# Kernel optimization log

Measured on AMD Instinct MI355X. Metric: run time of the kernel, lower is better.

Reference implementation:

```python
import jax, jax.numpy as jnp
import numpy as np

B = 262144
IN_F = 64
OUT_F = 64
HID = 256
QUAT_IDX = np.array([0, 1, 2, 3])
NON_QUAT_IDX = np.array(sorted(set(range(OUT_F)) - set(QUAT_IDX.tolist())))
TRIU_R, TRIU_C = np.triu_indices(4)  # row-major order, matches torch.triu_indices


def setup_inputs() -> dict:
    key = jax.random.key(0)
    k0, k1, k2 = jax.random.split(key, 3)
    z = jax.random.normal(k0, (B, IN_F), dtype=jnp.float32)
    W1 = jax.random.normal(k1, (IN_F, HID), dtype=jnp.float32) * (1.0 / np.sqrt(IN_F))
    b1 = jnp.zeros((HID,), dtype=jnp.float32)
    W2 = jax.random.normal(k2, (HID, OUT_F - 4), dtype=jnp.float32) * (1.0 / np.sqrt(HID))
    b2 = jnp.zeros((OUT_F - 4,), dtype=jnp.float32)
    return {"z": z, "W1": W1, "b1": b1, "W2": W2, "b2": b2}


def _recover_quat(z_v):
    # z_v: (B, 10) -> symmetric M: (B, 4, 4)
    n = z_v.shape[0]
    M = jnp.zeros((n, 4, 4), dtype=z_v.dtype)
    M = M.at[:, TRIU_R, TRIU_C].set(z_v)
    M = M.at[:, TRIU_C, TRIU_R].set(z_v)  # symmetrize (diagonal rewritten identically)
    _, vecs = jnp.linalg.eigh(M)  # ascending eigenvalues
    q = vecs[:, :, -1]            # eigenvector of largest eigenvalue, (B, 4)
    sign = jnp.sign(q[:, 0:1])
    sign = jnp.where(sign == 0, jnp.ones_like(sign), sign)
    sign = jax.lax.stop_gradient(sign)
    return q * sign


def reference(z, W1, b1, W2, b2):
    z2 = z.reshape(-1, z.shape[-1])
    q_pred = _recover_quat(z2[:, :10])
    h = jax.nn.relu(z2 @ W1 + b1)
    others_pred = h @ W2 + b2
    x = jnp.zeros((z2.shape[0], OUT_F), dtype=z2.dtype)
    x = x.at[:, QUAT_IDX].set(q_pred)
    x = x.at[:, NON_QUAT_IDX].set(others_pred)
    return x.reshape(*z.shape[:-1], OUT_F)
```

## Files before the change

kernel.cpp:

```cpp
#include <hip/hip_runtime.h>
#include <stdint.h>

#define NROWS 262144
#define INF   64
#define HIDN  256
#define OUTM  60
#define BLOCKS 512
#define BLOCK  1024

typedef __attribute__((ext_vector_type(8))) short bf16x8;
typedef __attribute__((ext_vector_type(4))) float f32x4;

__device__ __forceinline__ uint32_t pk2(float lo, float hi) {
  uint32_t r;
  asm("v_cvt_pk_bf16_f32 %0, %1, %2" : "=v"(r) : "v"(lo), "v"(hi));
  return r;
}

union U8 { uint32_t u[4]; bf16x8 v; uint4 q; };

__global__ __launch_bounds__(BLOCK, 1)
void veronese_fused(const float* __restrict__ z,  const float* __restrict__ W1,
                    const float* __restrict__ b1, const float* __restrict__ W2,
                    const float* __restrict__ b2, float* __restrict__ out) {
  __shared__ __align__(16) uint8_t lds[65536 + 8192];
  const int tid = threadIdx.x;

  {
    const int hid = tid & 255;
    const int q4  = tid >> 8;
    #pragma unroll
    for (int cc = 0; cc < 2; ++cc) {
      const int hc = q4 * 2 + cc;
      float f[8];
      #pragma unroll
      for (int j = 0; j < 8; ++j) f[j] = W1[(hc*8 + j) * HIDN + hid];
      U8 u;
      u.u[0] = pk2(f[0], f[1]); u.u[1] = pk2(f[2], f[3]);
      u.u[2] = pk2(f[4], f[5]); u.u[3] = pk2(f[6], f[7]);
      uint32_t off = (uint32_t)hid * 128 + (uint32_t)((hc * 16) ^ ((hid & 7) << 4));
      *reinterpret_cast<uint4*>(lds + off) = u.q;
    }
  }
  {
    const int o   = tid & 63;
    const int seg = tid >> 6;
    #pragma unroll
    for (int uu = 0; uu < 2; ++uu) {
      const int hb = seg * 16 + uu * 8;
      float f[8];
      #pragma unroll
      for (int j = 0; j < 8; ++j)
        f[j] = (o >= 4) ? W2[(hb + j) * OUTM + (o - 4)] : 0.0f;
      U8 u;
      u.u[0] = pk2(f[0], f[1]); u.u[1] = pk2(f[2], f[3]);
      u.u[2] = pk2(f[4], f[5]); u.u[3] = pk2(f[6], f[7]);
      uint32_t off = 32768u + (uint32_t)o * 512 + (uint32_t)((hb * 2) ^ ((o & 7) << 4));
      *reinterpret_cast<uint4*>(lds + off) = u.q;
    }
  }
  __syncthreads();

  const int l   = tid & 63;
  const int w   = tid >> 6;
  const int g   = l >> 4;
  const int l15 = l & 15;
  const uint32_t swz = (uint32_t)((l & 7) << 4);
  const int srcA = l15 + 32*(g & 1) + 16*(g >> 1);
  const int srcB = l15 + 32*(g & 1) + 16*(1 - (g >> 1));
  const bool hiq = (g & 2) != 0;
  const bool amI16 = (l & 16) != 0;

  f32x4 bias2[4];
  #pragma unroll
  for (int m = 0; m < 4; ++m) {
    int ob = 16*m + 4*g;
    if (ob >= 4) bias2[m] = *reinterpret_cast<const f32x4*>(b2 + ob - 4);
    else         bias2[m] = (f32x4){0.f, 0.f, 0.f, 0.f};
  }

  const int blockRow = blockIdx.x * (BLOCK / 2);
  const int rowBase  = blockRow + w * 32;

  bf16x8 zf[2][2];
  #pragma unroll
  for (int t = 0; t < 2; ++t) {
    const float* zp = z + (size_t)(rowBase + 16*t + l15) * INF;
    #pragma unroll
    for (int k1 = 0; k1 < 2; ++k1) {
      float4 a0 = *reinterpret_cast<const float4*>(zp + k1*32 + 8*g);
      float4 a1 = *reinterpret_cast<const float4*>(zp + k1*32 + 8*g + 4);
      U8 u;
      u.u[0] = pk2(a0.x, a0.y); u.u[1] = pk2(a0.z, a0.w);
      u.u[2] = pk2(a1.x, a1.y); u.u[3] = pk2(a1.z, a1.w);
      zf[t][k1] = u.v;
    }
  }

  if (w < 8) {
    const float* zq = z + (size_t)(blockRow + w * 64 + l) * INF;
    float4 qv0 = reinterpret_cast<const float4*>(zq)[0];
    float4 qv1 = reinterpret_cast<const float4*>(zq)[1];
    float4 qv2 = reinterpret_cast<const float4*>(zq)[2];
    float zv[10] = {qv0.x,qv0.y,qv0.z,qv0.w, qv1.x,qv1.y,qv1.z,qv1.w,
                    qv2.x,qv2.y};
    float M[4][4];
    M[0][0]=zv[0]; M[0][1]=zv[1]; M[0][2]=zv[2]; M[0][3]=zv[3];
    M[1][1]=zv[4]; M[1][2]=zv[5]; M[1][3]=zv[6];
    M[2][2]=zv[7]; M[2][3]=zv[8]; M[3][3]=zv[9];
    M[1][0]=zv[1]; M[2][0]=zv[2]; M[3][0]=zv[3];
    M[2][1]=zv[5]; M[3][1]=zv[6]; M[3][2]=zv[8];
    float V[4][4] = {{1.f,0.f,0.f,0.f},{0.f,1.f,0.f,0.f},
                     {0.f,0.f,1.f,0.f},{0.f,0.f,0.f,1.f}};

#define JROT(p, q) do {                                                      \
    float apq = M[p][q];                                                     \
    float app = M[p][p], aqq = M[q][q];                                      \
    float tau = (aqq - app) * (0.5f * __builtin_amdgcn_rcpf(apq));           \
    float t_r = copysignf(1.0f, tau) *                                       \
        __builtin_amdgcn_rcpf(fabsf(tau) +                                   \
            __builtin_amdgcn_sqrtf(fmaf(tau, tau, 1.0f)));                   \
    float t   = (fabsf(apq) > 1e-25f) ? t_r : 0.0f;                          \
    float c   = __builtin_amdgcn_rsqf(fmaf(t, t, 1.0f));                     \
    float s   = t * c;                                                       \
    M[p][p] = fmaf(-t, apq, app);                                            \
    M[q][q] = fmaf( t, apq, aqq);                                            \
    M[p][q] = 0.0f; M[q][p] = 0.0f;                                          \
    _Pragma("unroll")                                                        \
    for (int r = 0; r < 4; ++r) {                                            \
      if (r != p && r != q) {                                                \
        float arp = M[r][p], arq = M[r][q];                                  \
        float nrp = fmaf(-s, arq, c * arp);                                  \
        float nrq = fmaf( s, arp, c * arq);                                  \
        M[r][p] = nrp; M[p][r] = nrp;                                        \
        M[r][q] = nrq; M[q][r] = nrq;                                        \
      }                                                                      \
    }                                                                        \
    _Pragma("unroll")                                                        \
    for (int r = 0; r < 4; ++r) {                                            \
      float vrp = V[r][p], vrq = V[r][q];                                    \
      V[r][p] = fmaf(-s, vrq, c * vrp);                                      \
      V[r][q] = fmaf( s, vrp, c * vrq);                                      \
    }                                                                        \
  } while (0)

    #pragma unroll
    for (int sweep = 0; sweep < 6; ++sweep) {
      JROT(0, 1); JROT(0, 2); JROT(0, 3);
      JROT(1, 2); JROT(1, 3); JROT(2, 3);
    }
#undef JROT

    float bv = M[0][0];
    float q0 = V[0][0], q1 = V[1][0], q2 = V[2][0], q3 = V[3][0];
    #pragma unroll
    for (int j = 1; j < 4; ++j) {
      float dj = M[j][j];
      bool  b  = dj > bv;
      bv = b ? dj      : bv;
      q0 = b ? V[0][j] : q0;
      q1 = b ? V[1][j] : q1;
      q2 = b ? V[2][j] : q2;
      q3 = b ? V[3][j] : q3;
    }
    float sgn = (q0 < 0.0f) ? -1.0f : 1.0f;
    float4 qq = make_float4(q0*sgn, q1*sgn, q2*sgn, q3*sgn);
    *reinterpret_cast<float4*>(lds + 65536 + (uint32_t)(w*64 + l) * 16) = qq;
  }

  f32x4 acc2[2][4];
  #pragma unroll
  for (int t = 0; t < 2; ++t)
    #pragma unroll
    for (int m = 0; m < 4; ++m) acc2[t][m] = bias2[m];

  for (int ks = 0; ks < 8; ++ks) {
    uint32_t c[2][4];
    #pragma unroll
    for (int mm = 0; mm < 2; ++mm) {
      const int hb = 16*(2*ks + mm) + 4*g;
      f32x4 bv = *reinterpret_cast<const f32x4*>(b1 + hb);
      uint32_t rowb = (uint32_t)(16*(2*ks+mm) + l15) * 128;
      bf16x8 a0 = *reinterpret_cast<const bf16x8*>(
          lds + rowb + (((uint32_t)(16*g)) ^ swz));
      bf16x8 a1 = *reinterpret_cast<const bf16x8*>(
          lds + rowb + (((uint32_t)(64 + 16*g)) ^ swz));
      f32x4 acc1[2];
      __builtin_amdgcn_s_setprio(1);
      #pragma unroll
      for (int t = 0; t < 2; ++t) {
        acc1[t] = __builtin_amdgcn_mfma_f32_16x16x32_bf16(a0, zf[t][0], bv, 0,0,0);
        acc1[t] = __builtin_amdgcn_mfma_f32_16x16x32_bf16(a1, zf[t][1], acc1[t], 0,0,0);
      }
      __builtin_amdgcn_s_setprio(0);
      #pragma unroll
      for (int t = 0; t < 2; ++t) {
        float h0 = fmaxf(acc1[t][0], 0.f), h1 = fmaxf(acc1[t][1], 0.f);
        float h2 = fmaxf(acc1[t][2], 0.f), h3 = fmaxf(acc1[t][3], 0.f);
        c[t][2*mm+0] = pk2(h0, h1);
        c[t][2*mm+1] = pk2(h2, h3);
      }
    }
    bf16x8 a2[4];
    #pragma unroll
    for (int m = 0; m < 4; ++m) {
      uint32_t rowb = 32768u + (uint32_t)(16*m + l15) * 512;
      a2[m] = *reinterpret_cast<const bf16x8*>(
          lds + rowb + (((uint32_t)(64*ks + 16*g)) ^ swz));
    }
    #pragma unroll
    for (int t = 0; t < 2; ++t) {
      uint32_t v02a = amI16 ? c[t][2] : c[t][0];
      uint32_t v13a = amI16 ? c[t][3] : c[t][1];
      uint32_t v02b = amI16 ? c[t][0] : c[t][2];
      uint32_t v13b = amI16 ? c[t][1] : c[t][3];
      uint32_t s0 = (uint32_t)__shfl((int)v02a, srcA, 64);
      uint32_t s1 = (uint32_t)__shfl((int)v13a, srcA, 64);
      uint32_t s2 = (uint32_t)__shfl((int)v02b, srcB, 64);
      uint32_t s3 = (uint32_t)__shfl((int)v13b, srcB, 64);
      U8 bu;
      bu.u[0] = hiq ? s2 : s0;
      bu.u[1] = hiq ? s3 : s1;
      bu.u[2] = hiq ? s0 : s2;
      bu.u[3] = hiq ? s1 : s3;
      __builtin_amdgcn_s_setprio(1);
      #pragma unroll
      for (int m = 0; m < 4; ++m)
        acc2[t][m] = __builtin_amdgcn_mfma_f32_16x16x32_bf16(a2[m], bu.v, acc2[t][m], 0,0,0);
      __builtin_amdgcn_s_setprio(0);
    }
  }

  __syncthreads();
  #pragma unroll
  for (int t = 0; t < 2; ++t) {
    if (g == 0) {
      f32x4 qv = *reinterpret_cast<const f32x4*>(
          lds + 65536 + (uint32_t)(w*32 + 16*t + l15) * 16);
      acc2[t][0] = qv;
    }
  }

  #pragma unroll
  for (int t = 0; t < 2; ++t) {
    float* op = out + (size_t)(rowBase + 16*t + l15) * 64;
    #pragma unroll
    for (int m = 0; m < 4; ++m) {
      float4 v = make_float4(acc2[t][m][0], acc2[t][m][1],
                             acc2[t][m][2], acc2[t][m][3]);
      *reinterpret_cast<float4*>(op + 16*m + 4*g) = v;
    }
  }
}

extern "C" void kernel_launch(void* const* d_in, const int* in_sizes, int n_in,
                              void* d_out, int out_size, void* d_ws, size_t ws_size,
                              hipStream_t stream) {
  const float* z  = (const float*)d_in[0];
  const float* W1 = (const float*)d_in[1];
  const float* b1 = (const float*)d_in[2];
  const float* W2 = (const float*)d_in[3];
  const float* b2 = (const float*)d_in[4];
  float* out = (float*)d_out;

  hipLaunchKernelGGL(veronese_fused, dim3(BLOCKS), dim3(BLOCK), 0, stream,
                     z, W1, b1, W2, b2, out);
}
```

Before: 141.2 us.

## Split quaternion eigensolve into separate kernel and shrink MLP blocks for occupancy

Moves the per-row 4x4 Jacobi eigensolve out of the fused kernel into its own kernel, which writes quaternions to a workspace buffer. The MLP kernel then runs with 512-thread blocks, two blocks per CU and 64KB LDS, and reads the quaternions back from global memory. The aim is to remove the imbalance where only 8 of 16 waves ran the serial eigensolve while the rest waited at a barrier, and to raise occupancy. In exchange it adds a second launch, an extra global write and read of the quaternions, and a second read of z's first 10 columns, and each MLP block now loads and converts the weights for half as many rows.

```diff
diff --git a/kernel.cpp b/kernel.cpp
--- a/kernel.cpp
+++ b/kernel.cpp
@@ -5,8 +5,6 @@
 #define INF   64
 #define HIDN  256
 #define OUTM  60
-#define BLOCKS 512
-#define BLOCK  1024
 
 typedef __attribute__((ext_vector_type(8))) short bf16x8;
 typedef __attribute__((ext_vector_type(4))) float f32x4;
@@ -19,99 +17,23 @@
 
 union U8 { uint32_t u[4]; bf16x8 v; uint4 q; };
 
-__global__ __launch_bounds__(BLOCK, 1)
-void veronese_fused(const float* __restrict__ z,  const float* __restrict__ W1,
-                    const float* __restrict__ b1, const float* __restrict__ W2,
-                    const float* __restrict__ b2, float* __restrict__ out) {
-  __shared__ __align__(16) uint8_t lds[65536 + 8192];
-  const int tid = threadIdx.x;
-
-  {
-    const int hid = tid & 255;
-    const int q4  = tid >> 8;
-    #pragma unroll
-    for (int cc = 0; cc < 2; ++cc) {
-      const int hc = q4 * 2 + cc;
-      float f[8];
-      #pragma unroll
-      for (int j = 0; j < 8; ++j) f[j] = W1[(hc*8 + j) * HIDN + hid];
-      U8 u;
-      u.u[0] = pk2(f[0], f[1]); u.u[1] = pk2(f[2], f[3]);
-      u.u[2] = pk2(f[4], f[5]); u.u[3] = pk2(f[6], f[7]);
-      uint32_t off = (uint32_t)hid * 128 + (uint32_t)((hc * 16) ^ ((hid & 7) << 4));
-      *reinterpret_cast<uint4*>(lds + off) = u.q;
-    }
-  }
-  {
-    const int o   = tid & 63;
-    const int seg = tid >> 6;
-    #pragma unroll
-    for (int uu = 0; uu < 2; ++uu) {
-      const int hb = seg * 16 + uu * 8;
-      float f[8];
-      #pragma unroll
-      for (int j = 0; j < 8; ++j)
-        f[j] = (o >= 4) ? W2[(hb + j) * OUTM + (o - 4)] : 0.0f;
-      U8 u;
-      u.u[0] = pk2(f[0], f[1]); u.u[1] = pk2(f[2], f[3]);
-      u.u[2] = pk2(f[4], f[5]); u.u[3] = pk2(f[6], f[7]);
-      uint32_t off = 32768u + (uint32_t)o * 512 + (uint32_t)((hb * 2) ^ ((o & 7) << 4));
-      *reinterpret_cast<uint4*>(lds + off) = u.q;
-    }
-  }
-  __syncthreads();
-
-  const int l   = tid & 63;
-  const int w   = tid >> 6;
-  const int g   = l >> 4;
-  const int l15 = l & 15;
-  const uint32_t swz = (uint32_t)((l & 7) << 4);
-  const int srcA = l15 + 32*(g & 1) + 16*(g >> 1);
-  const int srcB = l15 + 32*(g & 1) + 16*(1 - (g >> 1));
-  const bool hiq = (g & 2) != 0;
-  const bool amI16 = (l & 16) != 0;
-
-  f32x4 bias2[4];
-  #pragma unroll
-  for (int m = 0; m < 4; ++m) {
-    int ob = 16*m + 4*g;
-    if (ob >= 4) bias2[m] = *reinterpret_cast<const f32x4*>(b2 + ob - 4);
-    else         bias2[m] = (f32x4){0.f, 0.f, 0.f, 0.f};
-  }
-
-  const int blockRow = blockIdx.x * (BLOCK / 2);
-  const int rowBase  = blockRow + w * 32;
-
-  bf16x8 zf[2][2];
-  #pragma unroll
-  for (int t = 0; t < 2; ++t) {
-    const float* zp = z + (size_t)(rowBase + 16*t + l15) * INF;
-    #pragma unroll
-    for (int k1 = 0; k1 < 2; ++k1) {
-      float4 a0 = *reinterpret_cast<const float4*>(zp + k1*32 + 8*g);
-      float4 a1 = *reinterpret_cast<const float4*>(zp + k1*32 + 8*g + 4);
-      U8 u;
-      u.u[0] = pk2(a0.x, a0.y); u.u[1] = pk2(a0.z, a0.w);
-      u.u[2] = pk2(a1.x, a1.y); u.u[3] = pk2(a1.z, a1.w);
-      zf[t][k1] = u.v;
-    }
-  }
-
-  if (w < 8) {
-    const float* zq = z + (size_t)(blockRow + w * 64 + l) * INF;
-    float4 qv0 = reinterpret_cast<const float4*>(zq)[0];
-    float4 qv1 = reinterpret_cast<const float4*>(zq)[1];
-    float4 qv2 = reinterpret_cast<const float4*>(zq)[2];
-    float zv[10] = {qv0.x,qv0.y,qv0.z,qv0.w, qv1.x,qv1.y,qv1.z,qv1.w,
-                    qv2.x,qv2.y};
-    float M[4][4];
-    M[0][0]=zv[0]; M[0][1]=zv[1]; M[0][2]=zv[2]; M[0][3]=zv[3];
-    M[1][1]=zv[4]; M[1][2]=zv[5]; M[1][3]=zv[6];
-    M[2][2]=zv[7]; M[2][3]=zv[8]; M[3][3]=zv[9];
-    M[1][0]=zv[1]; M[2][0]=zv[2]; M[3][0]=zv[3];
-    M[2][1]=zv[5]; M[3][1]=zv[6]; M[3][2]=zv[8];
-    float V[4][4] = {{1.f,0.f,0.f,0.f},{0.f,1.f,0.f,0.f},
-                     {0.f,0.f,1.f,0.f},{0.f,0.f,0.f,1.f}};
+__global__ __launch_bounds__(256)
+void veronese_quat(const float* __restrict__ z, float* __restrict__ ws) {
+  const int row = blockIdx.x * 256 + threadIdx.x;
+  const float* zr = z + (size_t)row * INF;
+  float4 v0 = reinterpret_cast<const float4*>(zr)[0];
+  float4 v1 = reinterpret_cast<const float4*>(zr)[1];
+  float2 v2 = *reinterpret_cast<const float2*>(zr + 8);
+  float zv[10] = {v0.x,v0.y,v0.z,v0.w, v1.x,v1.y,v1.z,v1.w, v2.x,v2.y};
+
+  float M[4][4];
+  M[0][0]=zv[0]; M[0][1]=zv[1]; M[0][2]=zv[2]; M[0][3]=zv[3];
+  M[1][1]=zv[4]; M[1][2]=zv[5]; M[1][3]=zv[6];
+  M[2][2]=zv[7]; M[2][3]=zv[8]; M[3][3]=zv[9];
+  M[1][0]=zv[1]; M[2][0]=zv[2]; M[3][0]=zv[3];
+  M[2][1]=zv[5]; M[3][1]=zv[6]; M[3][2]=zv[8];
+  float V[4][4] = {{1.f,0.f,0.f,0.f},{0.f,1.f,0.f,0.f},
+                   {0.f,0.f,1.f,0.f},{0.f,0.f,0.f,1.f}};
 
 #define JROT(p, q) do {                                                      \
     float apq = M[p][q];                                                     \
@@ -144,28 +66,106 @@
     }                                                                        \
   } while (0)
 
-    #pragma unroll
-    for (int sweep = 0; sweep < 6; ++sweep) {
-      JROT(0, 1); JROT(0, 2); JROT(0, 3);
-      JROT(1, 2); JROT(1, 3); JROT(2, 3);
-    }
+  #pragma unroll
+  for (int sweep = 0; sweep < 6; ++sweep) {
+    JROT(0, 1); JROT(0, 2); JROT(0, 3);
+    JROT(1, 2); JROT(1, 3); JROT(2, 3);
+  }
 #undef JROT
 
-    float bv = M[0][0];
-    float q0 = V[0][0], q1 = V[1][0], q2 = V[2][0], q3 = V[3][0];
-    #pragma unroll
-    for (int j = 1; j < 4; ++j) {
-      float dj = M[j][j];
-      bool  b  = dj > bv;
-      bv = b ? dj      : bv;
-      q0 = b ? V[0][j] : q0;
-      q1 = b ? V[1][j] : q1;
-      q2 = b ? V[2][j] : q2;
-      q3 = b ? V[3][j] : q3;
-    }
-    float sgn = (q0 < 0.0f) ? -1.0f : 1.0f;
-    float4 qq = make_float4(q0*sgn, q1*sgn, q2*sgn, q3*sgn);
-    *reinterpret_cast<float4*>(lds + 65536 + (uint32_t)(w*64 + l) * 16) = qq;
+  float bv = M[0][0];
+  float q0 = V[0][0], q1 = V[1][0], q2 = V[2][0], q3 = V[3][0];
+  #pragma unroll
+  for (int j = 1; j < 4; ++j) {
+    float dj = M[j][j];
+    bool  b  = dj > bv;
+    bv = b ? dj      : bv;
+    q0 = b ? V[0][j] : q0;
+    q1 = b ? V[1][j] : q1;
+    q2 = b ? V[2][j] : q2;
+    q3 = b ? V[3][j] : q3;
+  }
+  float sgn = (q0 < 0.0f) ? -1.0f : 1.0f;
+  float4 q = make_float4(q0*sgn, q1*sgn, q2*sgn, q3*sgn);
+  *reinterpret_cast<float4*>(ws + (size_t)row * 4) = q;
+}
+
+__global__ __launch_bounds__(512, 2)
+void veronese_mlp(const float* __restrict__ z,  const float* __restrict__ W1,
+                  const float* __restrict__ b1, const float* __restrict__ W2,
+                  const float* __restrict__ b2, const float* __restrict__ ws,
+                  float* __restrict__ out) {
+  __shared__ __align__(16) uint8_t lds[65536];
+  const int tid = threadIdx.x;
+
+  {
+    const int hid  = tid & 255;
+    const int half = tid >> 8;
+    #pragma unroll
+    for (int cc = 0; cc < 4; ++cc) {
+      const int hc = half * 4 + cc;
+      float f[8];
+      #pragma unroll
+      for (int j = 0; j < 8; ++j) f[j] = W1[(hc*8 + j) * HIDN + hid];
+      U8 u;
+      u.u[0] = pk2(f[0], f[1]); u.u[1] = pk2(f[2], f[3]);
+      u.u[2] = pk2(f[4], f[5]); u.u[3] = pk2(f[6], f[7]);
+      uint32_t off = (uint32_t)hid * 128 + (uint32_t)((hc * 16) ^ ((hid & 7) << 4));
+      *reinterpret_cast<uint4*>(lds + off) = u.q;
+    }
+  }
+  {
+    const int o   = tid & 63;
+    const int seg = tid >> 6;
+    #pragma unroll
+    for (int uu = 0; uu < 4; ++uu) {
+      const int hb = seg * 32 + uu * 8;
+      float f[8];
+      #pragma unroll
+      for (int j = 0; j < 8; ++j)
+        f[j] = (o >= 4) ? W2[(hb + j) * OUTM + (o - 4)] : 0.0f;
+      U8 u;
+      u.u[0] = pk2(f[0], f[1]); u.u[1] = pk2(f[2], f[3]);
+      u.u[2] = pk2(f[4], f[5]); u.u[3] = pk2(f[6], f[7]);
+      uint32_t off = 32768u + (uint32_t)o * 512 + (uint32_t)((hb * 2) ^ ((o & 7) << 4));
+      *reinterpret_cast<uint4*>(lds + off) = u.q;
+    }
+  }
+  __syncthreads();
+
+  const int l   = tid & 63;
+  const int w   = tid >> 6;
+  const int g   = l >> 4;
+  const int l15 = l & 15;
+  const uint32_t swz = (uint32_t)((l & 7) << 4);
+  const int srcA = l15 + 32*(g & 1) + 16*(g >> 1);
+  const int srcB = l15 + 32*(g & 1) + 16*(1 - (g >> 1));
+  const bool hiq = (g & 2) != 0;
+  const bool amI16 = (l & 16) != 0;
+
+  f32x4 bias2[4];
+  #pragma unroll
+  for (int m = 0; m < 4; ++m) {
+    int ob = 16*m + 4*g;
+    if (ob >= 4) bias2[m] = *reinterpret_cast<const f32x4*>(b2 + ob - 4);
+    else         bias2[m] = (f32x4){0.f, 0.f, 0.f, 0.f};
+  }
+
+  const int rowBase = blockIdx.x * 256 + w * 32;
+
+  bf16x8 zf[2][2];
+  #pragma unroll
+  for (int t = 0; t < 2; ++t) {
+    const float* zp = z + (size_t)(rowBase + 16*t + l15) * INF;
+    #pragma unroll
+    for (int k1 = 0; k1 < 2; ++k1) {
+      float4 a0 = *reinterpret_cast<const float4*>(zp + k1*32 + 8*g);
+      float4 a1 = *reinterpret_cast<const float4*>(zp + k1*32 + 8*g + 4);
+      U8 u;
+      u.u[0] = pk2(a0.x, a0.y); u.u[1] = pk2(a0.z, a0.w);
+      u.u[2] = pk2(a1.x, a1.y); u.u[3] = pk2(a1.z, a1.w);
+      zf[t][k1] = u.v;
+    }
   }
 
   f32x4 acc2[2][4];
@@ -231,12 +231,11 @@
     }
   }
 
-  __syncthreads();
   #pragma unroll
   for (int t = 0; t < 2; ++t) {
     if (g == 0) {
-      f32x4 qv = *reinterpret_cast<const f32x4*>(
-          lds + 65536 + (uint32_t)(w*32 + 16*t + l15) * 16);
+      const int row = rowBase + 16*t + l15;
+      f32x4 qv = *reinterpret_cast<const f32x4*>(ws + (size_t)row * 4);
       acc2[t][0] = qv;
     }
   }
@@ -261,8 +260,11 @@
   const float* b1 = (const float*)d_in[2];
   const float* W2 = (const float*)d_in[3];
   const float* b2 = (const float*)d_in[4];
+  float* ws  = (float*)d_ws;
   float* out = (float*)d_out;
 
-  hipLaunchKernelGGL(veronese_fused, dim3(BLOCKS), dim3(BLOCK), 0, stream,
-                     z, W1, b1, W2, b2, out);
-}
+  hipLaunchKernelGGL(veronese_quat, dim3(NROWS / 256), dim3(256), 0, stream,
+                     z, ws);
+  hipLaunchKernelGGL(veronese_mlp, dim3(NROWS / 256), dim3(512), 0, stream,
+                     z, W1, b1, W2, b2, ws, out);
+}
```

New measurement: 152.6 us. +8.1%, slower.
